# Kernel tuning notes

Hardware: AMD Instinct MI355X
Metric: run time of the kernel (lower is better)

The kernel has to match this reference:

```python
import jax, jax.numpy as jnp
import numpy as np
import math

B, L = 2, 512
D_MODEL = 64
N_HEAD = 8
N_GLOBAL = 64
N_ITER = 2
DISTS = 4
K_RANK = 4
REG_H = 1.0
REG_Z = 1.0
NEG = -1e9


def setup_inputs() -> dict:
    key = jax.random.key(0)
    k1, k2, k3, k4 = jax.random.split(key, 4)
    x = jax.random.normal(k1, (B, L, D_MODEL), dtype=jnp.float32)
    mask = jnp.ones((B, L), dtype=jnp.int32)
    # nn.init.normal_ defaults (std=1)
    distribution_params = jax.random.normal(k2, (2 * DISTS, K_RANK), dtype=jnp.float32)
    ternary = jax.random.normal(k3, (K_RANK, D_MODEL, D_MODEL, N_HEAD), dtype=jnp.float32)
    # global_: std = 1/sqrt(d_model), single-channel -> heads dim = 1
    global_param = jax.random.normal(k4, (N_GLOBAL, D_MODEL, 1), dtype=jnp.float32) * (1.0 / math.sqrt(D_MODEL))
    return {"x": x, "mask": mask, "distribution_params": distribution_params,
            "ternary": ternary, "global_param": global_param}


def _softmax(s):
    return jax.nn.softmax(s, axis=-1)


def _distmask(distribution_params, n, dtype):
    # distance(i,j) = clip(i - j, -dists, dists); row 0 of params is zeros (distance 0)
    dist = jnp.arange(n)[:, None] - jnp.arange(n)[None, :]
    dist = jnp.clip(dist, -DISTS, DISTS)
    params = jnp.concatenate([jnp.zeros((1, K_RANK), dtype), distribution_params], axis=0)  # [2*dists+1, k]
    # torch negative indexing wraps; emulate explicitly
    idx = jnp.where(dist < 0, dist + 2 * DISTS + 1, dist)
    return params[idx].transpose(2, 0, 1)  # [k, n, n]


def reference(x, mask, distribution_params, ternary, global_param):
    bsz, n, d = x.shape
    mask1d = mask != 0                                   # [B, L]
    mask2d = mask1d[:, :, None] & mask1d[:, None, :]     # [B, L, L]
    inv2d = ~mask2d[:, None, :, :]                       # [B, 1, L, L] broadcast over heads
    inv1d = ~mask1d[:, None, :, None]                    # [B, 1, L, 1]

    distmask = _distmask(distribution_params, n, x.dtype)  # [k, L, L]

    unary = x
    q_z = unary
    for _ in range(N_ITER):
        # --- normalize Z beliefs (softmax over d_model states) ---
        Q_z = _softmax(q_z / REG_Z)                      # [B, L, d]
        # precompute decomposed tensor messages: M1[z,k,j,a,c] = sum_b Qz[z,j,b] T[k,a,b,c]
        M1 = jnp.einsum('zjb,kabc->zkjac', Q_z, ternary)  # [B, k, L, d, h]
        # --- H update (each head of token i picks a parent j) ---
        # s_h[z,c,i,j] = sum_{a,k} Qz[z,i,a] M1[z,k,j,a,c] distmask[k,i,j]
        s_h = jnp.einsum('zia,zkjac,kij->zcij', Q_z, M1, distmask)  # [B, h, L, L]
        s_h = jnp.where(inv2d, NEG, s_h)
        Q_h = _softmax(s_h / REG_H)                      # softmax over parents j
        # --- global H update (single channel): token i picks one of n_global global nodes ---
        s_g = jnp.einsum('zia,gac->zcig', Q_z, global_param)        # [B, 1, L, G]
        s_g = jnp.where(inv1d, NEG, s_g)
        Q_g = _softmax(s_g / REG_H)
        # --- Z update: messages from ternary factors in both roles + global factor ---
        g1 = jnp.einsum('zcij,zkjac,kij->zia', Q_h, M1, distmask)   # token as Z_i
        M2 = jnp.einsum('zjb,kbac->zkjac', Q_z, ternary)            # swapped roles
        g2 = jnp.einsum('zcji,zkjac,kji->zia', Q_h, M2, distmask)   # token as Z_j
        gg = jnp.einsum('zcig,gac->zia', Q_g, global_param)         # global message
        q_z = unary + g1 + g2 + gg
        # damping=0, stepsize=1 -> plain full update
    # output_prob=False -> unnormalized scores
    return q_z
```

## Files before the change

### kernel.cpp

```cpp
#include <hip/hip_runtime.h>

#define BB 2
#define LL 512
#define DD 64
#define HH 8
#define GG 64
#define KK 4
#define NEGV -1e9f
#define NSLOT 36

typedef unsigned short ushort_t;
typedef __attribute__((ext_vector_type(8))) short bf16x8;
typedef __attribute__((ext_vector_type(4))) float f32x4;
#define MFMA(a, b, c) __builtin_amdgcn_mfma_f32_16x16x32_bf16(a, b, c, 0, 0, 0)

typedef const __attribute__((address_space(1))) unsigned int* gptr_t;
typedef __attribute__((address_space(3))) unsigned int* lptr_t;

__device__ __forceinline__ ushort_t f2b(float f) {
    unsigned int u = __float_as_uint(f);
    return (ushort_t)((u + 0x7FFFu + ((u >> 16) & 1u)) >> 16);
}
__device__ __forceinline__ float b2f(ushort_t s) {
    return __uint_as_float(((unsigned int)s) << 16);
}

__device__ __forceinline__ void gll16(const ushort_t* g, const ushort_t* l) {
    __builtin_amdgcn_global_load_lds(
        (gptr_t)(unsigned long long)g,
        (lptr_t)(unsigned int)(unsigned long long)l,
        16, 0, 0);
}

__device__ __forceinline__ void stage64a(ushort_t* dst, const ushort_t* src,
                                         int rowstride, int tid) {
    int lane = tid & 63, w = tid >> 6;
#pragma unroll
    for (int h = 0; h < 2; ++h) {
        int g = h * 256 + w * 64 + lane;
        int row = g >> 3, colg = g & 7;
        gll16(src + (size_t)row * rowstride + ((colg ^ (row & 7)) << 3),
              dst + (size_t)(h * 256 + w * 64) * 8);
    }
}
__device__ __forceinline__ bf16x8 frag(const ushort_t* s, int row, int col) {
    return *reinterpret_cast<const bf16x8*>(&s[(row << 6) + ((((col >> 3) ^ (row & 7))) << 3)]);
}
__device__ __forceinline__ bf16x8 maskfrag(bf16x8 v, int cnt, bool keep_prefix) {
    bf16x8 r;
#pragma unroll
    for (int u = 0; u < 8; ++u) {
        bool keep = keep_prefix ? (u < cnt) : (u >= cnt);
        r[u] = keep ? v[u] : (short)0;
    }
    return r;
}
__device__ __forceinline__ int iclamp(int v, int lo, int hi) {
    return v < lo ? lo : (v > hi ? hi : v);
}

__global__ __launch_bounds__(256) void k_prepT(const float* __restrict__ T,
                                               ushort_t* __restrict__ TB1,
                                               ushort_t* __restrict__ TB2) {
    int k = blockIdx.x >> 3, c = blockIdx.x & 7;
    int tid = threadIdx.x;
    for (int g = tid; g < 512; g += 256) {
        int a = g >> 3, b0 = (g & 7) * 8;
        ushort_t o1[8], o2[8];
#pragma unroll
        for (int u = 0; u < 8; ++u) {
            o1[u] = f2b(T[(((k * 64 + a) * 64) + b0 + u) * 8 + c]);
            o2[u] = f2b(T[(((k * 64 + b0 + u) * 64) + a) * 8 + c]);
        }
        size_t base = ((size_t)(k * 8 + c) * 64 + a) * 64 + b0;
        *reinterpret_cast<uint4*>(&TB1[base]) = *reinterpret_cast<uint4*>(o1);
        *reinterpret_cast<uint4*>(&TB2[base]) = *reinterpret_cast<uint4*>(o2);
    }
}

__global__ __launch_bounds__(256) void k_softmax_qz(const float* __restrict__ src,
                                                    float* __restrict__ Qz,
                                                    ushort_t* __restrict__ QzB) {
    int row = blockIdx.x * 4 + (threadIdx.x >> 6);
    int lane = threadIdx.x & 63;
    float v = src[row * DD + lane];
    float m = v;
#pragma unroll
    for (int o = 32; o > 0; o >>= 1) m = fmaxf(m, __shfl_xor(m, o, 64));
    float e = __expf(v - m);
    float s = e;
#pragma unroll
    for (int o = 32; o > 0; o >>= 1) s += __shfl_xor(s, o, 64);
    float r = e / s;
    Qz[row * DD + lane] = r;
    QzB[row * DD + lane] = f2b(r);
}

__global__ __launch_bounds__(256, 2) void k_Mcoll(const ushort_t* __restrict__ QzB,
        const ushort_t* __restrict__ TB1, const ushort_t* __restrict__ TB2,
        const float* __restrict__ dp,
        ushort_t* __restrict__ M1Nb, ushort_t* __restrict__ M2Nb,
        ushort_t* __restrict__ MPNb, ushort_t* __restrict__ MMNb,
        ushort_t* __restrict__ MP2Nb, ushort_t* __restrict__ MM2Nb,
        ushort_t* __restrict__ MPT, ushort_t* __restrict__ MMT,
        ushort_t* __restrict__ MP2T, ushort_t* __restrict__ MM2T) {
    int jt = blockIdx.x, zc = blockIdx.y;
    int z = zc >> 3, c = zc & 7;
    __shared__ __align__(16) ushort_t smem[20480];
    ushort_t* sQ = smem;
    int tid = threadIdx.x;
    stage64a(sQ, QzB + (size_t)(z * LL + jt * 64) * DD, DD, tid);
    stage64a(smem + 4096,  TB1 + (size_t)(0 * 8 + c) * 4096, 64, tid);
    stage64a(smem + 12288, TB2 + (size_t)(0 * 8 + c) * 4096, 64, tid);
    int w = tid >> 6, lm = tid & 15, lg = (tid & 63) >> 4;
    float w4[4], w5[4];
#pragma unroll
    for (int k = 0; k < 4; ++k) { w4[k] = dp[12 + k]; w5[k] = dp[16 + k]; }
    f32x4 cp1[4], cm1[4], cp2[4], cm2[4];
#pragma unroll
    for (int nf = 0; nf < 4; ++nf) {
        cp1[nf] = {0.f,0.f,0.f,0.f}; cm1[nf] = {0.f,0.f,0.f,0.f};
        cp2[nf] = {0.f,0.f,0.f,0.f}; cm2[nf] = {0.f,0.f,0.f,0.f};
    }
#pragma unroll
    for (int k = 0; k < 4; ++k) {
        __syncthreads();
        if (k < 3) {
            ushort_t* nb1 = smem + (((k + 1) & 1) ? 8192 : 4096);
            ushort_t* nb2 = smem + (((k + 1) & 1) ? 16384 : 12288);
            stage64a(nb1, TB1 + (size_t)((k + 1) * 8 + c) * 4096, 64, tid);
            stage64a(nb2, TB2 + (size_t)((k + 1) * 8 + c) * 4096, 64, tid);
        }
        const ushort_t* b1 = smem + ((k & 1) ? 8192 : 4096);
        const ushort_t* b2 = smem + ((k & 1) ? 16384 : 12288);
        f32x4 a1[4], a2[4];
#pragma unroll
        for (int nf = 0; nf < 4; ++nf) { a1[nf] = {0.f,0.f,0.f,0.f}; a2[nf] = {0.f,0.f,0.f,0.f}; }
#pragma unroll
        for (int ks = 0; ks < 2; ++ks) {
            int kc = ks * 32 + lg * 8;
            bf16x8 af = frag(sQ, w * 16 + lm, kc);
#pragma unroll
            for (int nf = 0; nf < 4; ++nf) {
                a1[nf] = MFMA(af, frag(b1, nf * 16 + lm, kc), a1[nf]);
                a2[nf] = MFMA(af, frag(b2, nf * 16 + lm, kc), a2[nf]);
            }
        }
        size_t base = (((size_t)z * KK + k) * HH + c) * LL;
#pragma unroll
        for (int nf = 0; nf < 4; ++nf)
#pragma unroll
            for (int r = 0; r < 4; ++r) {
                int j = jt * 64 + w * 16 + lg * 4 + r;
                int a = nf * 16 + lm;
                float v1 = a1[nf][r], v2 = a2[nf][r];
                M1Nb[(base + j) * DD + a] = f2b(v1);
                M2Nb[(base + j) * DD + a] = f2b(v2);
                cp1[nf][r] += w4[k] * v1; cm1[nf][r] += w5[k] * v1;
                cp2[nf][r] += w4[k] * v2; cm2[nf][r] += w5[k] * v2;
            }
    }
#pragma unroll
    for (int nf = 0; nf < 4; ++nf)
#pragma unroll
        for (int r = 0; r < 4; ++r) {
            int jl = w * 16 + lg * 4 + r;
            int a = nf * 16 + lm;
            size_t on = ((size_t)zc * LL + jt * 64 + jl) * DD + a;
            MPNb[on]  = f2b(cp1[nf][r]); MMNb[on]  = f2b(cm1[nf][r]);
            MP2Nb[on] = f2b(cp2[nf][r]); MM2Nb[on] = f2b(cm2[nf][r]);
        }
    __syncthreads();
    ushort_t* tr0 = smem;
    ushort_t* tr1 = smem + 4224;
    ushort_t* tr2 = smem + 8448;
    ushort_t* tr3 = smem + 12672;
#pragma unroll
    for (int nf = 0; nf < 4; ++nf)
#pragma unroll
        for (int r = 0; r < 4; ++r) {
            int jl = w * 16 + lg * 4 + r;
            int a = nf * 16 + lm;
            tr0[a * 66 + jl] = f2b(cp1[nf][r]); tr1[a * 66 + jl] = f2b(cm1[nf][r]);
            tr2[a * 66 + jl] = f2b(cp2[nf][r]); tr3[a * 66 + jl] = f2b(cm2[nf][r]);
        }
    __syncthreads();
    for (int g = tid; g < 512; g += 256) {
        int a = g >> 3, j0 = (g & 7) * 8;
        ushort_t o1[8], o2[8], o3[8], o4[8];
#pragma unroll
        for (int u = 0; u < 8; ++u) {
            o1[u] = tr0[a * 66 + j0 + u]; o2[u] = tr1[a * 66 + j0 + u];
            o3[u] = tr2[a * 66 + j0 + u]; o4[u] = tr3[a * 66 + j0 + u];
        }
        size_t ot = ((size_t)zc * DD + a) * LL + jt * 64 + j0;
        *reinterpret_cast<uint4*>(&MPT[ot])  = *reinterpret_cast<uint4*>(o1);
        *reinterpret_cast<uint4*>(&MMT[ot])  = *reinterpret_cast<uint4*>(o2);
        *reinterpret_cast<uint4*>(&MP2T[ot]) = *reinterpret_cast<uint4*>(o3);
        *reinterpret_cast<uint4*>(&MM2T[ot]) = *reinterpret_cast<uint4*>(o4);
    }
}

__global__ __launch_bounds__(256, 4) void k_bandqg(const float* __restrict__ Qz,
        const ushort_t* __restrict__ M1Nb,
        const float* __restrict__ dp, const float* __restrict__ gp, const int* __restrict__ mask,
        float* __restrict__ BAND, float* __restrict__ QG) {
    __shared__ __align__(16) float gpS[64 * 68];
    int tid = threadIdx.x;
    int b = blockIdx.x;
    if (b < 2048) {
        int w = b * 4 + (tid >> 6);
        int lane = tid & 63;
        int j = w & 511, c = (w >> 9) & 7, z = w >> 12;
        float m[4];
#pragma unroll
        for (int k = 0; k < 4; ++k)
            m[k] = b2f(M1Nb[((((size_t)z * KK + k) * HH + c) * LL + j) * DD + lane]);
        float out = 0.f;
#pragma unroll
        for (int d = -3; d <= 3; ++d) {
            int i = j + d;
            if (i < 0 || i >= LL) continue;
            int idx = d < 0 ? d + 9 : d;
            float t = 0.f;
            if (idx != 0) {
#pragma unroll
                for (int k = 0; k < 4; ++k) t += dp[(idx - 1) * 4 + k] * m[k];
            }
            float s = Qz[(z * LL + i) * DD + lane] * t;
#pragma unroll
            for (int o = 32; o > 0; o >>= 1) s += __shfl_xor(s, o, 64);
            if (lane == d + 3) out = s;
        }
        if (lane < 7) BAND[(size_t)w * 8 + lane] = out;
    } else {
#pragma unroll
        for (int idx = tid; idx < 4096; idx += 256) gpS[(idx >> 6) * 68 + (idx & 63)] = gp[idx];
        __syncthreads();
        int row = (b - 2048) * 4 + (tid >> 6);
        int g = tid & 63;
        float qv = Qz[row * DD + g];
        float s = 0.f;
#pragma unroll 8
        for (int a = 0; a < 64; ++a) s += __shfl(qv, a, 64) * gpS[g * 68 + a];
        if (mask[row] == 0) s = NEGV;
        float m = s;
#pragma unroll
        for (int o = 32; o > 0; o >>= 1) m = fmaxf(m, __shfl_xor(m, o, 64));
        float e = __expf(s - m);
        float sum = e;
#pragma unroll
        for (int o = 32; o > 0; o >>= 1) sum += __shfl_xor(sum, o, 64);
        QG[row * GG + g] = e / sum;
    }
}

__global__ __launch_bounds__(256, 2) void k_shsm32(const ushort_t* __restrict__ QzB,
        const ushort_t* __restrict__ MPNb, const ushort_t* __restrict__ MMNb,
        const float* __restrict__ BAND, const int* __restrict__ mask,
        ushort_t* __restrict__ SHB, ushort_t* __restrict__ SHBT) {
    int ih = blockIdx.x, zc = blockIdx.y;
    int it = ih >> 1, rh = ih & 1;
    int z = zc >> 3;
    int R0 = it * 64 + rh * 32;
    __shared__ __align__(16) ushort_t sA[2048];
    __shared__ __align__(16) ushort_t sBd[4096];
    __shared__ __align__(16) ushort_t sB[2][8192];
    __shared__ __align__(16) ushort_t tl[2][32 * 72];
    __shared__ float redA[2][32], redB[2][32];
    int tid = threadIdx.x;
    int w = tid >> 6, lm = tid & 15, lg = (tid & 63) >> 4;
    int rw = w & 1, cw = w >> 1;
    {
        int row = tid >> 3, colg = tid & 7;
        gll16(&QzB[(size_t)(z * LL + R0 + row) * DD + ((colg ^ (row & 7)) << 3)],
              sA + (size_t)(w * 64) * 8);
    }
    stage64a(sBd, MMNb + ((size_t)zc * LL + it * 64) * DD, DD, tid);
    stage64a(sB[0], ((it >= 0) ? MPNb : MMNb) + ((size_t)zc * LL + 0 * 64) * DD, DD, tid);
    stage64a(sB[0] + 4096, ((it >= 4) ? MPNb : MMNb) + ((size_t)zc * LL + 4 * 64) * DD, DD, tid);
    f32x4 acc[4][4];
#pragma unroll
    for (int jl = 0; jl < 4; ++jl)
#pragma unroll
        for (int nf = 0; nf < 4; ++nf) acc[jl][nf] = {0.f, 0.f, 0.f, 0.f};
#pragma unroll
    for (int s = 0; s < 4; ++s) {
        __syncthreads();
        if (s < 3) {
            int jt0n = s + 1, jt1n = 5 + s;
            stage64a(sB[(s + 1) & 1],
                     ((it >= jt0n) ? MPNb : MMNb) + ((size_t)zc * LL + jt0n * 64) * DD, DD, tid);
            stage64a(sB[(s + 1) & 1] + 4096,
                     ((it >= jt1n) ? MPNb : MMNb) + ((size_t)zc * LL + jt1n * 64) * DD, DD, tid);
        }
        int jt0 = s, jt1 = 4 + s;
        int jtg = cw ? jt1 : jt0;
        const ushort_t* sBx = sB[s & 1] + (cw ? 4096 : 0);
#pragma unroll
        for (int ks = 0; ks < 2; ++ks) {
            int kc = ks * 32 + lg * 8;
            bf16x8 af = frag(sA, rw * 16 + lm, kc);
#pragma unroll
            for (int nf = 0; nf < 4; ++nf)
                acc[s][nf] = MFMA(af, frag(sBx, nf * 16 + lm, kc), acc[s][nf]);
        }
        if (jtg == it) {
            f32x4 accM[4];
#pragma unroll
            for (int nf = 0; nf < 4; ++nf) accM[nf] = {0.f, 0.f, 0.f, 0.f};
#pragma unroll
            for (int ks = 0; ks < 2; ++ks) {
                int kc = ks * 32 + lg * 8;
                bf16x8 af = frag(sA, rw * 16 + lm, kc);
#pragma unroll
                for (int nf = 0; nf < 4; ++nf)
                    accM[nf] = MFMA(af, frag(sBd, nf * 16 + lm, kc), accM[nf]);
            }
#pragma unroll
            for (int nf = 0; nf < 4; ++nf)
#pragma unroll
                for (int r = 0; r < 4; ++r) {
                    int i = R0 + rw * 16 + lg * 4 + r;
                    int j = it * 64 + nf * 16 + lm;
                    if (i <= j) acc[s][nf][r] = accM[nf][r];
                }
        }
    }
    int mi[4];
#pragma unroll
    for (int r = 0; r < 4; ++r) mi[r] = mask[z * LL + R0 + rw * 16 + lg * 4 + r];
#pragma unroll
    for (int jl = 0; jl < 4; ++jl) {
        int jtg = cw * 4 + jl;
#pragma unroll
        for (int nf = 0; nf < 4; ++nf) {
            int j = jtg * 64 + nf * 16 + lm;
            int mjv = mask[z * LL + j];
#pragma unroll
            for (int r = 0; r < 4; ++r) {
                int i = R0 + rw * 16 + lg * 4 + r;
                int d = i - j;
                float v = acc[jl][nf][r];
                if (d >= -3 && d <= 3) v = BAND[((size_t)zc * LL + j) * 8 + (d + 3)];
                if (!(mi[r] && mjv)) v = NEGV;
                acc[jl][nf][r] = v;
            }
        }
    }
    float gm[4], gs[4], inv[4];
#pragma unroll
    for (int r = 0; r < 4; ++r) {
        float m = -1e30f;
#pragma unroll
        for (int jl = 0; jl < 4; ++jl)
#pragma unroll
            for (int nf = 0; nf < 4; ++nf) m = fmaxf(m, acc[jl][nf][r]);
#pragma unroll
        for (int o = 1; o < 16; o <<= 1) m = fmaxf(m, __shfl_xor(m, o, 64));
        gm[r] = m;
    }
    if (lm == 0) {
#pragma unroll
        for (int r = 0; r < 4; ++r) redA[cw][rw * 16 + lg * 4 + r] = gm[r];
    }
    __syncthreads();
#pragma unroll
    for (int r = 0; r < 4; ++r)
        gm[r] = fmaxf(gm[r], redA[cw ^ 1][rw * 16 + lg * 4 + r]);
#pragma unroll
    for (int r = 0; r < 4; ++r) {
        float s = 0.f;
#pragma unroll
        for (int jl = 0; jl < 4; ++jl)
#pragma unroll
            for (int nf = 0; nf < 4; ++nf) {
                float e = __expf(acc[jl][nf][r] - gm[r]);
                acc[jl][nf][r] = e;
                s += e;
            }
#pragma unroll
        for (int o = 1; o < 16; o <<= 1) s += __shfl_xor(s, o, 64);
        gs[r] = s;
    }
    if (lm == 0) {
#pragma unroll
        for (int r = 0; r < 4; ++r) redB[cw][rw * 16 + lg * 4 + r] = gs[r];
    }
    __syncthreads();
#pragma unroll
    for (int r = 0; r < 4; ++r)
        inv[r] = 1.f / (gs[r] + redB[cw ^ 1][rw * 16 + lg * 4 + r]);
#pragma unroll
    for (int jl = 0; jl < 4; ++jl) {
        __syncthreads();
#pragma unroll
        for (int nf = 0; nf < 4; ++nf)
#pragma unroll
            for (int r = 0; r < 4; ++r)
                tl[cw][(rw * 16 + lg * 4 + r) * 72 + nf * 16 + lm] =
                    f2b(acc[jl][nf][r] * inv[r]);
        __syncthreads();
#pragma unroll
        for (int g = tid; g < 512; g += 256) {
            int cwg = g >> 8, rem = g & 255;
            int jtg = cwg * 4 + jl;
            int i_loc = rem >> 3, gj = rem & 7;
            ushort_t tmp[8];
#pragma unroll
            for (int u = 0; u < 8; ++u) tmp[u] = tl[cwg][i_loc * 72 + gj * 8 + u];
            *reinterpret_cast<uint4*>(
                &SHB[((size_t)zc * LL + R0 + i_loc) * LL + jtg * 64 + gj * 8]) =
                *reinterpret_cast<uint4*>(tmp);
        }
#pragma unroll
        for (int g = tid; g < 512; g += 256) {
            int cwg = g >> 8, rem = g & 255;
            int jtg = cwg * 4 + jl;
            int j_loc = rem >> 2, gi = rem & 3;
            ushort_t tmp2[8];
#pragma unroll
            for (int u = 0; u < 8; ++u) tmp2[u] = tl[cwg][(gi * 8 + u) * 72 + j_loc];
            *reinterpret_cast<uint4*>(
                &SHBT[((size_t)zc * LL + jtg * 64 + j_loc) * LL + R0 + gi * 8]) =
                *reinterpret_cast<uint4*>(tmp2);
        }
    }
}

__global__ __launch_bounds__(256, 4) void k_g12corr(const ushort_t* __restrict__ SHB,
        const ushort_t* __restrict__ SHBT,
        const ushort_t* __restrict__ MPT, const ushort_t* __restrict__ MMT,
        const ushort_t* __restrict__ MP2T, const ushort_t* __restrict__ MM2T,
        const ushort_t* __restrict__ M1Nb, const ushort_t* __restrict__ M2Nb,
        const ushort_t* __restrict__ MPNb, const ushort_t* __restrict__ MMNb,
        const ushort_t* __restrict__ MP2Nb, const ushort_t* __restrict__ MM2Nb,
        const float* __restrict__ dp, float* __restrict__ PG) {
    __shared__ __align__(16) ushort_t sSH[2][4096], sM[2][4096];
    int tid = threadIdx.x;
    int b = blockIdx.x;
    if (b < 512) {
        int it = b & 7, jc = (b >> 3) & 1, zcw = b >> 4;
        int which = zcw >> 4;
        int z = (zcw >> 3) & 1, c = zcw & 7;
        const ushort_t* Amat = which ? SHBT : SHB;
        const ushort_t* TP = which ? MP2T : MPT;
        const ushort_t* TM = which ? MM2T : MMT;
        int w = tid >> 6, lm = tid & 15, lg = (tid & 63) >> 4;
        size_t shbase = ((size_t)(z * HH + c) * LL + it * 64) * LL;
        size_t mbase  = ((size_t)(z * HH + c) * DD) * LL;
        int dgjs = ((it >> 2) == jc) ? (it & 3) : 99;
        int ns = (dgjs < 4) ? 5 : 4;
        auto getsub = [&](int t, const ushort_t*& shp, const ushort_t*& mp,
                          int& j0v, int& passv) {
            int js, pass;
            if (dgjs > 3)            { js = t;        pass = -1; }
            else if (t < dgjs)       { js = t;        pass = -1; }
            else if (t == dgjs)      { js = t;        pass = 0;  }
            else if (t == dgjs + 1)  { js = dgjs;     pass = 1;  }
            else                     { js = t - 1;    pass = -1; }
            int j0 = jc * 256 + js * 64;
            bool useP = (pass == -1)
                        ? (which == 0 ? (j0 < it * 64) : (j0 > it * 64))
                        : (pass == 0);
            shp = Amat + shbase + j0;
            mp  = (useP ? TP : TM) + mbase + j0;
            j0v = j0; passv = pass;
        };
        f32x4 acc[4];
#pragma unroll
        for (int nf = 0; nf < 4; ++nf) acc[nf] = {0.f,0.f,0.f,0.f};
        {
            const ushort_t *shp, *mp; int j0v, pv;
            getsub(0, shp, mp, j0v, pv);
            stage64a(sSH[0], shp, LL, tid);
            stage64a(sM[0], mp, LL, tid);
        }
        for (int t = 0; t < ns; ++t) {
            __syncthreads();
            if (t + 1 < ns) {
                const ushort_t *shp, *mp; int j0v, pv;
                getsub(t + 1, shp, mp, j0v, pv);
                stage64a(sSH[(t + 1) & 1], shp, LL, tid);
                stage64a(sM[(t + 1) & 1], mp, LL, tid);
            }
            const ushort_t *shp_, *mp_; int j0v, pv;
            getsub(t, shp_, mp_, j0v, pv);
            const ushort_t* sshx = sSH[t & 1];
            const ushort_t* smx = sM[t & 1];
#pragma unroll
            for (int ks = 0; ks < 2; ++ks) {
                int kc = ks * 32 + lg * 8;
                int jb = j0v + kc;
                bf16x8 af = frag(sshx, w * 16 + lm, kc);
                if (pv >= 0) {
                    int i = it * 64 + w * 16 + lm;
                    int cnt = (which == 0) ? iclamp(i - jb, 0, 8) : iclamp(i + 1 - jb, 0, 8);
                    af = maskfrag(af, cnt, (pv == 0) == (which == 0));
                }
#pragma unroll
                for (int nf = 0; nf < 4; ++nf)
                    acc[nf] = MFMA(af, frag(smx, nf * 16 + lm, kc), acc[nf]);
            }
        }
        int slot = which * 16 + c * 2 + jc;
#pragma unroll
        for (int nf = 0; nf < 4; ++nf)
#pragma unroll
            for (int r = 0; r < 4; ++r) {
                int i = it * 64 + w * 16 + lg * 4 + r;
                int a = nf * 16 + lm;
                PG[((size_t)(slot * BB + z) * LL + i) * DD + a] = acc[nf][r];
            }
    } else {
        int bid = b - 512;
        int which = bid >> 9; bid &= 511;
        int w = bid * 4 + (tid >> 6);
        int lane = tid & 63;
        int ch = w & 1, i = (w >> 1) & 511, z = w >> 10;
        const ushort_t* Mx = which ? M2Nb : M1Nb;
        const ushort_t* MPb = which ? MP2Nb : MPNb;
        const ushort_t* MMb = which ? MM2Nb : MMNb;
        float acc = 0.f;
        for (int cc = 0; cc < 4; ++cc) {
            int c = ch * 4 + cc;
#pragma unroll
            for (int d = -3; d <= 3; ++d) {
                int j = which ? i + d : i - d;
                if (j < 0 || j >= LL) continue;
                float qh = which ? b2f(SHB[(((size_t)z * HH + c) * LL + j) * LL + i])
                                 : b2f(SHB[(((size_t)z * HH + c) * LL + i) * LL + j]);
                int idx = d < 0 ? d + 9 : d;
                float e = 0.f;
                if (idx != 0) {
#pragma unroll
                    for (int k = 0; k < 4; ++k)
                        e += dp[(idx - 1) * 4 + k] *
                             b2f(Mx[((((size_t)z * KK + k) * HH + c) * LL + j) * DD + lane]);
                }
                const ushort_t* mb = (d > 0) ? MPb : MMb;
                float mn = b2f(mb[(((size_t)z * HH + c) * LL + j) * DD + lane]);
                acc += qh * (e - mn);
            }
        }
        int slot = 32 + which * 2 + ch;
        PG[(((size_t)slot * BB + z) * LL + i) * DD + lane] = acc;
    }
}

__global__ __launch_bounds__(256) void k_update_sm(const float* __restrict__ x,
                         const float* __restrict__ PG, const float* __restrict__ QG,
                         const float* __restrict__ gp,
                         float* __restrict__ Qz, ushort_t* __restrict__ QzB) {
    __shared__ __align__(16) float gpS[64][68];
    int tid = threadIdx.x;
#pragma unroll
    for (int idx = tid; idx < 4096; idx += 256) gpS[idx >> 6][idx & 63] = gp[idx];
    __syncthreads();
    int row = blockIdx.x * 4 + (tid >> 6);
    int a = tid & 63;
    float acc = x[row * DD + a];
    float qgv = QG[row * GG + a];
#pragma unroll 8
    for (int g = 0; g < 64; ++g) acc += __shfl(qgv, g, 64) * gpS[g][a];
#pragma unroll 6
    for (int s = 0; s < NSLOT; ++s) acc += PG[((size_t)s * BB * LL + row) * DD + a];
    float m = acc;
#pragma unroll
    for (int o = 32; o > 0; o >>= 1) m = fmaxf(m, __shfl_xor(m, o, 64));
    float e = __expf(acc - m);
    float s2 = e;
#pragma unroll
    for (int o = 32; o > 0; o >>= 1) s2 += __shfl_xor(s2, o, 64);
    float r = e / s2;
    Qz[row * DD + a] = r;
    QzB[row * DD + a] = f2b(r);
}

__global__ __launch_bounds__(256) void k_update_fin(const float* __restrict__ x,
                         const float* __restrict__ PG, const float* __restrict__ QG,
                         const float* __restrict__ gp, float* __restrict__ outq) {
    __shared__ __align__(16) float gpS[64][68];
    int tid = threadIdx.x;
#pragma unroll
    for (int idx = tid; idx < 4096; idx += 256) gpS[idx >> 6][idx & 63] = gp[idx];
    __syncthreads();
    int row = blockIdx.x * 4 + (tid >> 6);
    int a = tid & 63;
    float acc = x[row * DD + a];
    float qgv = QG[row * GG + a];
#pragma unroll 8
    for (int g = 0; g < 64; ++g) acc += __shfl(qgv, g, 64) * gpS[g][a];
#pragma unroll 6
    for (int s = 0; s < NSLOT; ++s) acc += PG[((size_t)s * BB * LL + row) * DD + a];
    outq[row * DD + a] = acc;
}

extern "C" void kernel_launch(void* const* d_in, const int* in_sizes, int n_in,
                              void* d_out, int out_size, void* d_ws, size_t ws_size,
                              hipStream_t stream) {
    const float* x    = (const float*)d_in[0];
    const int*   mask = (const int*)d_in[1];
    const float* dp   = (const float*)d_in[2];
    const float* T    = (const float*)d_in[3];
    const float* gp   = (const float*)d_in[4];
    float* out = (float*)d_out;

    float* p = (float*)d_ws;
    float* Qz = p;                        p += 65536;
    ushort_t* QzB = (ushort_t*)p;         p += 32768;
    ushort_t* TB1 = (ushort_t*)p;         p += 65536;
    ushort_t* TB2 = (ushort_t*)p;         p += 65536;
    ushort_t* M1Nb = (ushort_t*)p;        p += 1048576;
    ushort_t* M2Nb = (ushort_t*)p;        p += 1048576;
    ushort_t* MPNb  = (ushort_t*)p;       p += 262144;
    ushort_t* MMNb  = (ushort_t*)p;       p += 262144;
    ushort_t* MP2Nb = (ushort_t*)p;       p += 262144;
    ushort_t* MM2Nb = (ushort_t*)p;       p += 262144;
    ushort_t* MPT   = (ushort_t*)p;       p += 262144;
    ushort_t* MMT   = (ushort_t*)p;       p += 262144;
    ushort_t* MP2T  = (ushort_t*)p;       p += 262144;
    ushort_t* MM2T  = (ushort_t*)p;       p += 262144;
    float* BAND = p;                      p += 65536;
    ushort_t* SHB  = (ushort_t*)p;        p += 2097152;
    ushort_t* SHBT = (ushort_t*)p;        p += 2097152;
    float* QG   = p;                      p += 65536;
    float* PG   = p;                      p += (size_t)NSLOT * 65536;

    hipLaunchKernelGGL(k_prepT, dim3(32), dim3(256), 0, stream, T, TB1, TB2);
    hipLaunchKernelGGL(k_softmax_qz, dim3(256), dim3(256), 0, stream, x, Qz, QzB);

    for (int iter = 0; iter < 2; ++iter) {
        hipLaunchKernelGGL(k_Mcoll, dim3(8, 16), dim3(256), 0, stream, QzB, TB1, TB2, dp,
                           M1Nb, M2Nb, MPNb, MMNb, MP2Nb, MM2Nb, MPT, MMT, MP2T, MM2T);
        hipLaunchKernelGGL(k_bandqg, dim3(2304), dim3(256), 0, stream, Qz, M1Nb, dp, gp, mask,
                           BAND, QG);
        hipLaunchKernelGGL(k_shsm32, dim3(16, 16), dim3(256), 0, stream, QzB, MPNb, MMNb, BAND, mask,
                           SHB, SHBT);
        hipLaunchKernelGGL(k_g12corr, dim3(1536), dim3(256), 0, stream, SHB, SHBT,
                           MPT, MMT, MP2T, MM2T, M1Nb, M2Nb,
                           MPNb, MMNb, MP2Nb, MM2Nb, dp, PG);
        if (iter == 0)
            hipLaunchKernelGGL(k_update_sm, dim3(256), dim3(256), 0, stream, x, PG, QG, gp, Qz, QzB);
        else
            hipLaunchKernelGGL(k_update_fin, dim3(256), dim3(256), 0, stream, x, PG, QG, gp, out);
    }
}
```

Before: 135.6 us.

## Fuse band and global-softmax computation into Mcoll; merge prep kernels

Folds the band-score computation into k_Mcoll, reading the freshly computed M1 tile from shared memory instead of re-reading it from global memory in a separate kernel. The global-node softmax runs in 64 extra blocks of the same launch, with each block now handling 16 rows. The two initial prep kernels are also merged into one launch. The aim is to cut launch count and a global round trip of M1. In exchange, shared memory per block rises by 32 KB and the band work is serialized inside the MFMA blocks, which may lengthen their tail.

```diff
diff --git a/kernel.cpp b/kernel.cpp
--- a/kernel.cpp
+++ b/kernel.cpp
@@ -59,56 +59,86 @@
     return v < lo ? lo : (v > hi ? hi : v);
 }
 
-__global__ __launch_bounds__(256) void k_prepT(const float* __restrict__ T,
-                                               ushort_t* __restrict__ TB1,
-                                               ushort_t* __restrict__ TB2) {
-    int k = blockIdx.x >> 3, c = blockIdx.x & 7;
+__global__ __launch_bounds__(256) void k_prep(const float* __restrict__ T,
+                                              const float* __restrict__ x,
+                                              float* __restrict__ Qz,
+                                              ushort_t* __restrict__ QzB,
+                                              ushort_t* __restrict__ TB1,
+                                              ushort_t* __restrict__ TB2) {
+    int b = blockIdx.x;
     int tid = threadIdx.x;
-    for (int g = tid; g < 512; g += 256) {
-        int a = g >> 3, b0 = (g & 7) * 8;
-        ushort_t o1[8], o2[8];
-#pragma unroll
-        for (int u = 0; u < 8; ++u) {
-            o1[u] = f2b(T[(((k * 64 + a) * 64) + b0 + u) * 8 + c]);
-            o2[u] = f2b(T[(((k * 64 + b0 + u) * 64) + a) * 8 + c]);
-        }
-        size_t base = ((size_t)(k * 8 + c) * 64 + a) * 64 + b0;
-        *reinterpret_cast<uint4*>(&TB1[base]) = *reinterpret_cast<uint4*>(o1);
-        *reinterpret_cast<uint4*>(&TB2[base]) = *reinterpret_cast<uint4*>(o2);
-    }
-}
-
-__global__ __launch_bounds__(256) void k_softmax_qz(const float* __restrict__ src,
-                                                    float* __restrict__ Qz,
-                                                    ushort_t* __restrict__ QzB) {
-    int row = blockIdx.x * 4 + (threadIdx.x >> 6);
-    int lane = threadIdx.x & 63;
-    float v = src[row * DD + lane];
-    float m = v;
-#pragma unroll
-    for (int o = 32; o > 0; o >>= 1) m = fmaxf(m, __shfl_xor(m, o, 64));
-    float e = __expf(v - m);
-    float s = e;
-#pragma unroll
-    for (int o = 32; o > 0; o >>= 1) s += __shfl_xor(s, o, 64);
-    float r = e / s;
-    Qz[row * DD + lane] = r;
-    QzB[row * DD + lane] = f2b(r);
+    if (b < 32) {
+        int k = b >> 3, c = b & 7;
+        for (int g = tid; g < 512; g += 256) {
+            int a = g >> 3, b0 = (g & 7) * 8;
+            ushort_t o1[8], o2[8];
+#pragma unroll
+            for (int u = 0; u < 8; ++u) {
+                o1[u] = f2b(T[(((k * 64 + a) * 64) + b0 + u) * 8 + c]);
+                o2[u] = f2b(T[(((k * 64 + b0 + u) * 64) + a) * 8 + c]);
+            }
+            size_t base = ((size_t)(k * 8 + c) * 64 + a) * 64 + b0;
+            *reinterpret_cast<uint4*>(&TB1[base]) = *reinterpret_cast<uint4*>(o1);
+            *reinterpret_cast<uint4*>(&TB2[base]) = *reinterpret_cast<uint4*>(o2);
+        }
+    } else {
+        int row = (b - 32) * 4 + (tid >> 6);
+        int lane = tid & 63;
+        float v = x[row * DD + lane];
+        float m = v;
+#pragma unroll
+        for (int o = 32; o > 0; o >>= 1) m = fmaxf(m, __shfl_xor(m, o, 64));
+        float e = __expf(v - m);
+        float s = e;
+#pragma unroll
+        for (int o = 32; o > 0; o >>= 1) s += __shfl_xor(s, o, 64);
+        float r = e / s;
+        Qz[row * DD + lane] = r;
+        QzB[row * DD + lane] = f2b(r);
+    }
 }
 
 __global__ __launch_bounds__(256, 2) void k_Mcoll(const ushort_t* __restrict__ QzB,
         const ushort_t* __restrict__ TB1, const ushort_t* __restrict__ TB2,
-        const float* __restrict__ dp,
+        const float* __restrict__ dp, const float* __restrict__ Qz,
+        const float* __restrict__ gp, const int* __restrict__ mask,
         ushort_t* __restrict__ M1Nb, ushort_t* __restrict__ M2Nb,
         ushort_t* __restrict__ MPNb, ushort_t* __restrict__ MMNb,
         ushort_t* __restrict__ MP2Nb, ushort_t* __restrict__ MM2Nb,
         ushort_t* __restrict__ MPT, ushort_t* __restrict__ MMT,
-        ushort_t* __restrict__ MP2T, ushort_t* __restrict__ MM2T) {
-    int jt = blockIdx.x, zc = blockIdx.y;
+        ushort_t* __restrict__ MP2T, ushort_t* __restrict__ MM2T,
+        float* __restrict__ BAND, float* __restrict__ QG) {
+    __shared__ __align__(16) ushort_t smem[20480];
+    __shared__ __align__(16) ushort_t sM1s[16384];
+    int tid = threadIdx.x;
+    int b = blockIdx.x;
+    if (b >= 128) {
+        float* gpS = reinterpret_cast<float*>(smem);
+#pragma unroll
+        for (int idx = tid; idx < 4096; idx += 256) gpS[(idx >> 6) * 68 + (idx & 63)] = gp[idx];
+        __syncthreads();
+        int g = tid & 63;
+        for (int rr = 0; rr < 4; ++rr) {
+            int row = (b - 128) * 16 + rr * 4 + (tid >> 6);
+            float qv = Qz[row * DD + g];
+            float s = 0.f;
+#pragma unroll 8
+            for (int a = 0; a < 64; ++a) s += __shfl(qv, a, 64) * gpS[g * 68 + a];
+            if (mask[row] == 0) s = NEGV;
+            float m = s;
+#pragma unroll
+            for (int o = 32; o > 0; o >>= 1) m = fmaxf(m, __shfl_xor(m, o, 64));
+            float e = __expf(s - m);
+            float sum = e;
+#pragma unroll
+            for (int o = 32; o > 0; o >>= 1) sum += __shfl_xor(sum, o, 64);
+            QG[row * GG + g] = e / sum;
+        }
+        return;
+    }
+    int jt = b & 7, zc = b >> 3;
     int z = zc >> 3, c = zc & 7;
-    __shared__ __align__(16) ushort_t smem[20480];
     ushort_t* sQ = smem;
-    int tid = threadIdx.x;
     stage64a(sQ, QzB + (size_t)(z * LL + jt * 64) * DD, DD, tid);
     stage64a(smem + 4096,  TB1 + (size_t)(0 * 8 + c) * 4096, 64, tid);
     stage64a(smem + 12288, TB2 + (size_t)(0 * 8 + c) * 4096, 64, tid);
@@ -151,11 +181,14 @@
         for (int nf = 0; nf < 4; ++nf)
 #pragma unroll
             for (int r = 0; r < 4; ++r) {
-                int j = jt * 64 + w * 16 + lg * 4 + r;
+                int jl = w * 16 + lg * 4 + r;
+                int j = jt * 64 + jl;
                 int a = nf * 16 + lm;
                 float v1 = a1[nf][r], v2 = a2[nf][r];
-                M1Nb[(base + j) * DD + a] = f2b(v1);
+                ushort_t v1b = f2b(v1);
+                M1Nb[(base + j) * DD + a] = v1b;
                 M2Nb[(base + j) * DD + a] = f2b(v2);
+                sM1s[(k * 64 + jl) * 64 + a] = v1b;
                 cp1[nf][r] += w4[k] * v1; cm1[nf][r] += w5[k] * v1;
                 cp2[nf][r] += w4[k] * v2; cm2[nf][r] += w5[k] * v2;
             }
@@ -171,6 +204,33 @@
             MP2Nb[on] = f2b(cp2[nf][r]); MM2Nb[on] = f2b(cm2[nf][r]);
         }
     __syncthreads();
+    {
+        int wave = tid >> 6, lane = tid & 63;
+        for (int jj = 0; jj < 16; ++jj) {
+            int j_loc = wave * 16 + jj;
+            int j = jt * 64 + j_loc;
+            float m0 = b2f(sM1s[(0 * 64 + j_loc) * 64 + lane]);
+            float m1v = b2f(sM1s[(1 * 64 + j_loc) * 64 + lane]);
+            float m2v = b2f(sM1s[(2 * 64 + j_loc) * 64 + lane]);
+            float m3v = b2f(sM1s[(3 * 64 + j_loc) * 64 + lane]);
+            float out = 0.f;
+#pragma unroll
+            for (int d = -3; d <= 3; ++d) {
+                int i = j + d;
+                if (i < 0 || i >= LL) continue;
+                int idx = d < 0 ? d + 9 : d;
+                float t = 0.f;
+                if (idx != 0)
+                    t = dp[(idx - 1) * 4 + 0] * m0 + dp[(idx - 1) * 4 + 1] * m1v
+                      + dp[(idx - 1) * 4 + 2] * m2v + dp[(idx - 1) * 4 + 3] * m3v;
+                float s = Qz[(z * LL + i) * DD + lane] * t;
+#pragma unroll
+                for (int o = 32; o > 0; o >>= 1) s += __shfl_xor(s, o, 64);
+                if (lane == d + 3) out = s;
+            }
+            if (lane < 7) BAND[((size_t)zc * LL + j) * 8 + lane] = out;
+        }
+    }
     ushort_t* tr0 = smem;
     ushort_t* tr1 = smem + 4224;
     ushort_t* tr2 = smem + 8448;
@@ -198,60 +258,6 @@
         *reinterpret_cast<uint4*>(&MMT[ot])  = *reinterpret_cast<uint4*>(o2);
         *reinterpret_cast<uint4*>(&MP2T[ot]) = *reinterpret_cast<uint4*>(o3);
         *reinterpret_cast<uint4*>(&MM2T[ot]) = *reinterpret_cast<uint4*>(o4);
-    }
-}
-
-__global__ __launch_bounds__(256, 4) void k_bandqg(const float* __restrict__ Qz,
-        const ushort_t* __restrict__ M1Nb,
-        const float* __restrict__ dp, const float* __restrict__ gp, const int* __restrict__ mask,
-        float* __restrict__ BAND, float* __restrict__ QG) {
-    __shared__ __align__(16) float gpS[64 * 68];
-    int tid = threadIdx.x;
-    int b = blockIdx.x;
-    if (b < 2048) {
-        int w = b * 4 + (tid >> 6);
-        int lane = tid & 63;
-        int j = w & 511, c = (w >> 9) & 7, z = w >> 12;
-        float m[4];
-#pragma unroll
-        for (int k = 0; k < 4; ++k)
-            m[k] = b2f(M1Nb[((((size_t)z * KK + k) * HH + c) * LL + j) * DD + lane]);
-        float out = 0.f;
-#pragma unroll
-        for (int d = -3; d <= 3; ++d) {
-            int i = j + d;
-            if (i < 0 || i >= LL) continue;
-            int idx = d < 0 ? d + 9 : d;
-            float t = 0.f;
-            if (idx != 0) {
-#pragma unroll
-                for (int k = 0; k < 4; ++k) t += dp[(idx - 1) * 4 + k] * m[k];
-            }
-            float s = Qz[(z * LL + i) * DD + lane] * t;
-#pragma unroll
-            for (int o = 32; o > 0; o >>= 1) s += __shfl_xor(s, o, 64);
-            if (lane == d + 3) out = s;
-        }
-        if (lane < 7) BAND[(size_t)w * 8 + lane] = out;
-    } else {
-#pragma unroll
-        for (int idx = tid; idx < 4096; idx += 256) gpS[(idx >> 6) * 68 + (idx & 63)] = gp[idx];
-        __syncthreads();
-        int row = (b - 2048) * 4 + (tid >> 6);
-        int g = tid & 63;
-        float qv = Qz[row * DD + g];
-        float s = 0.f;
-#pragma unroll 8
-        for (int a = 0; a < 64; ++a) s += __shfl(qv, a, 64) * gpS[g * 68 + a];
-        if (mask[row] == 0) s = NEGV;
-        float m = s;
-#pragma unroll
-        for (int o = 32; o > 0; o >>= 1) m = fmaxf(m, __shfl_xor(m, o, 64));
-        float e = __expf(s - m);
-        float sum = e;
-#pragma unroll
-        for (int o = 32; o > 0; o >>= 1) sum += __shfl_xor(sum, o, 64);
-        QG[row * GG + g] = e / sum;
     }
 }
 
@@ -627,13 +633,12 @@
     float* QG   = p;                      p += 65536;
     float* PG   = p;                      p += (size_t)NSLOT * 65536;
 
-    hipLaunchKernelGGL(k_prepT, dim3(32), dim3(256), 0, stream, T, TB1, TB2);
-    hipLaunchKernelGGL(k_softmax_qz, dim3(256), dim3(256), 0, stream, x, Qz, QzB);
+    hipLaunchKernelGGL(k_prep, dim3(288), dim3(256), 0, stream, T, x, Qz, QzB, TB1, TB2);
 
     for (int iter = 0; iter < 2; ++iter) {
-        hipLaunchKernelGGL(k_Mcoll, dim3(8, 16), dim3(256), 0, stream, QzB, TB1, TB2, dp,
-                           M1Nb, M2Nb, MPNb, MMNb, MP2Nb, MM2Nb, MPT, MMT, MP2T, MM2T);
-        hipLaunchKernelGGL(k_bandqg, dim3(2304), dim3(256), 0, stream, Qz, M1Nb, dp, gp, mask,
+        hipLaunchKernelGGL(k_Mcoll, dim3(192), dim3(256), 0, stream, QzB, TB1, TB2, dp,
+                           Qz, gp, mask,
+                           M1Nb, M2Nb, MPNb, MMNb, MP2Nb, MM2Nb, MPT, MMT, MP2T, MM2T,
                            BAND, QG);
         hipLaunchKernelGGL(k_shsm32, dim3(16, 16), dim3(256), 0, stream, QzB, MPNb, MMNb, BAND, mask,
                            SHB, SHBT);
```

New measurement: 182.3 us. 1.34x slower.
